# Kernel tuning notes

Hardware: AMD Instinct MI355X
Metric: run time of the kernel (lower is better)

## Reference

```python
import jax, jax.numpy as jnp
import numpy as np

DIM = 1024
N_HEADS = 16
HEAD_DIM = DIM // N_HEADS
MAX_CTX = 2048


def build_rope_cache(seq_len, head_dim, base=10000.0):
    inv_freq = 1.0 / (base ** (jnp.arange(0, head_dim, 2, dtype=jnp.float32) / head_dim))
    t = jnp.arange(seq_len, dtype=jnp.float32)
    freqs = jnp.einsum('i,j->ij', t, inv_freq)  # [T, head_dim//2]
    return jnp.cos(freqs), jnp.sin(freqs)


def apply_rope(x, cos, sin):
    # x: [B, H, T, D]; interleaved even/odd rotation
    x1 = x[..., 0::2]
    x2 = x[..., 1::2]
    c = cos[None, None, :x.shape[-2], :]
    s = sin[None, None, :x.shape[-2], :]
    rx1 = x1 * c - x2 * s
    rx2 = x1 * s + x2 * c
    return jnp.stack([rx1, rx2], axis=-1).reshape(x.shape)


def setup_inputs() -> dict:
    key = jax.random.key(0)
    k1, k2, k3 = jax.random.split(key, 3)
    B, T = 2, 2048
    x = jax.random.normal(k1, (B, T, DIM), dtype=jnp.float32)
    # torch nn.Linear weight shapes: [out_features, in_features]
    qkv_w = jax.random.normal(k2, (3 * DIM, DIM), dtype=jnp.float32) * (1.0 / np.sqrt(DIM))
    out_w = jax.random.normal(k3, (DIM, DIM), dtype=jnp.float32) * (1.0 / np.sqrt(DIM))
    return {"x": x, "qkv_w": qkv_w, "out_w": out_w}


def reference(x, qkv_w, out_w):
    B, T, C = x.shape
    cos, sin = build_rope_cache(MAX_CTX, HEAD_DIM)
    cos = cos.astype(x.dtype)
    sin = sin.astype(x.dtype)

    qkv = jnp.einsum('btc,dc->btd', x, qkv_w)  # [B, T, 3C]
    qkv = qkv.reshape(B, T, 3, N_HEADS, HEAD_DIM).transpose(2, 0, 3, 1, 4)
    q, k, v = qkv[0], qkv[1], qkv[2]  # each [B, H, T, D]

    q = apply_rope(q, cos, sin)
    k = apply_rope(k, cos, sin)

    scale = 1.0 / np.sqrt(HEAD_DIM)
    scores = jnp.einsum('bhqd,bhkd->bhqk', q, k) * scale  # [B, H, T, T]
    causal = jnp.tril(jnp.ones((T, T), dtype=bool))
    scores = jnp.where(causal[None, None], scores, jnp.finfo(scores.dtype).min)
    attn = jax.nn.softmax(scores, axis=-1)
    y = jnp.einsum('bhqk,bhkd->bhqd', attn, v)  # [B, H, T, D]
    y = y.transpose(0, 2, 1, 3).reshape(B, T, C)
    return jnp.einsum('btc,dc->btd', y, out_w)
```

## Files before the change

kernel.cpp:

```cpp
#include <hip/hip_runtime.h>
#include <hip/hip_bf16.h>
#include <cstdint>
#include <cstddef>

#define B_SZ   2
#define T_CTX  2048
#define DIM_C  1024
#define NHEAD  16
#define HD     64
#define NBH    (B_SZ*NHEAD)

typedef __attribute__((ext_vector_type(8))) short short8;
typedef __attribute__((ext_vector_type(4))) float f32x4;
typedef __attribute__((ext_vector_type(16))) float f32x16;

union BV8 { short8 s; __hip_bfloat16 h[8]; unsigned short u[8]; };
union U32x4 { uint32_t u[4]; short8 s8; };

#define GLD16(gp, lp) \
  __builtin_amdgcn_global_load_lds((const __attribute__((address_space(1))) void*)(gp), \
                                   (__attribute__((address_space(3))) void*)(lp), 16, 0, 0)

__device__ inline uint32_t pkbf(float a, float b) {
  union { __hip_bfloat16 h; unsigned short u; } ua, ub;
  ua.h = __float2bfloat16(a);
  ub.h = __float2bfloat16(b);
  return ((uint32_t)ub.u << 16) | (uint32_t)ua.u;
}

__global__ __launch_bounds__(256) void cvt_all(const float* __restrict__ x,
                                               const float* __restrict__ wq,
                                               const float* __restrict__ wo,
                                               __hip_bfloat16* __restrict__ xb,
                                               __hip_bfloat16* __restrict__ wqb,
                                               __hip_bfloat16* __restrict__ wob) {
  int i = blockIdx.x * 256 + threadIdx.x;
  const float* src;
  __hip_bfloat16* dst;
  int off;
  if (i < 1048576) { src = x; dst = xb; off = i; }
  else if (i < 1835008) { src = wq; dst = wqb; off = i - 1048576; }
  else { src = wo; dst = wob; off = i - 1835008; }
  float4 v = reinterpret_cast<const float4*>(src)[off];
  BV8 o;
  o.h[0] = __float2bfloat16(v.x);
  o.h[1] = __float2bfloat16(v.y);
  o.h[2] = __float2bfloat16(v.z);
  o.h[3] = __float2bfloat16(v.w);
  ushort4 st = { o.u[0], o.u[1], o.u[2], o.u[3] };
  reinterpret_cast<ushort4*>(dst)[off] = st;
}

template <typename OutT>
__global__ __launch_bounds__(256) void gemm_bt(const __hip_bfloat16* __restrict__ A,
                                               const __hip_bfloat16* __restrict__ Bt,
                                               OutT* __restrict__ C,
                                               int M, int N, int K) {
  __shared__ __align__(16) char smem[65536];
  const int tid = threadIdx.x;
  const int w = tid >> 6, l = tid & 63;
  const int l15 = l & 15, l4 = l >> 4;
  const int wr = w >> 1, wc = w & 1;
  const int gx = (int)gridDim.x;
  const int nwg = gx * (int)gridDim.y;
  int lin = (int)blockIdx.y * gx + (int)blockIdx.x;
  lin = (lin & 7) * (nwg >> 3) + (lin >> 3);
  const long bm = (long)(lin / gx) * 128;
  const long bn = (long)(lin % gx) * 128;

  f32x4 acc[4][4] = {};

  const int srow = tid >> 3;
  const int scol = (tid & 7) * 16;
  const int ssw  = scol ^ ((srow & 7) << 4);
  const char* Ab  = (const char*)A;
  const char* Btb = (const char*)Bt;

#define GSTAGE(kt_, buf_)                                                   \
  {                                                                         \
    char* base_ = smem + (buf_) * 32768;                                    \
    _Pragma("unroll")                                                       \
    for (int it = 0; it < 4; ++it) {                                        \
      long arow = bm + it * 32 + srow;                                      \
      GLD16(Ab + (arow * K + (kt_)) * 2 + ssw, base_ + it * 4096 + w * 1024);            \
      long brow = bn + it * 32 + srow;                                      \
      GLD16(Btb + (brow * K + (kt_)) * 2 + ssw, base_ + 16384 + it * 4096 + w * 1024);   \
    }                                                                       \
  }

  GSTAGE(0, 0)

  int cur = 0;
  for (int kt = 0; kt < K; kt += 64) {
    __syncthreads();
    if (kt + 64 < K) GSTAGE(kt + 64, cur ^ 1)
    const char* Ac = smem + cur * 32768;
    const char* Bc = Ac + 16384;
#pragma unroll
    for (int ksub = 0; ksub < 2; ++ksub) {
      short8 aF[4], bF[4];
#pragma unroll
      for (int m = 0; m < 4; ++m) {
        int R = wr * 64 + m * 16 + l15;
        aF[m] = *(const short8*)(Ac + R * 128 + ((ksub * 64 + l4 * 16) ^ ((R & 7) << 4)));
      }
#pragma unroll
      for (int n = 0; n < 4; ++n) {
        int R = wc * 64 + n * 16 + l15;
        bF[n] = *(const short8*)(Bc + R * 128 + ((ksub * 64 + l4 * 16) ^ ((R & 7) << 4)));
      }
#pragma unroll
      for (int m = 0; m < 4; ++m)
#pragma unroll
        for (int n = 0; n < 4; ++n)
          acc[m][n] = __builtin_amdgcn_mfma_f32_16x16x32_bf16(aF[m], bF[n], acc[m][n], 0, 0, 0);
    }
    cur ^= 1;
  }
#undef GSTAGE

#pragma unroll
  for (int m = 0; m < 4; ++m)
#pragma unroll
    for (int n = 0; n < 4; ++n)
#pragma unroll
      for (int r = 0; r < 4; ++r) {
        long row = bm + wr * 64 + m * 16 + l4 * 4 + r;
        long col = bn + wc * 64 + n * 16 + l15;
        float v = acc[m][n][r];
        if constexpr (sizeof(OutT) == 2) {
          C[row * N + col] = __float2bfloat16(v);
        } else {
          C[row * N + col] = v;
        }
      }
}

__global__ __launch_bounds__(256) void rope_pack(const __hip_bfloat16* __restrict__ qkv,
                                                 __hip_bfloat16* __restrict__ Qb,
                                                 __hip_bfloat16* __restrict__ Kb,
                                                 __hip_bfloat16* __restrict__ VTb) {
  __shared__ __hip_bfloat16 vt[64][72];
  const int bh = blockIdx.x;
  const int b = bh >> 4, h = bh & 15;
  const int t0 = blockIdx.y * 64;
  const int tid = threadIdx.x;
  const float QSCL = 0.125f * 1.4426950408889634f;

#pragma unroll
  for (int rep = 0; rep < 2; ++rep) {
    int idx = rep * 256 + tid;
    int tt = idx >> 3;
    int d0 = (idx & 7) * 8;
    int t = t0 + tt;
    size_t src = ((size_t)(b * T_CTX + t)) * 3072 + h * 64 + d0;
    BV8 qv, kv, vv, qo, ko;
    qv.s = *(const short8*)(qkv + src);
    kv.s = *(const short8*)(qkv + src + 1024);
    vv.s = *(const short8*)(qkv + src + 2048);
#pragma unroll
    for (int p = 0; p < 4; ++p) {
      int i = (d0 >> 1) + p;
      float inv = exp2f(-13.287712379549449f * ((float)(2 * i) * (1.0f / 64.0f)));
      float ang = (float)t * inv;
      float sn, cn;
      sincosf(ang, &sn, &cn);
      float q1 = __bfloat162float(qv.h[2 * p]);
      float q2 = __bfloat162float(qv.h[2 * p + 1]);
      float k1 = __bfloat162float(kv.h[2 * p]);
      float k2 = __bfloat162float(kv.h[2 * p + 1]);
      qo.h[2 * p]     = __float2bfloat16((q1 * cn - q2 * sn) * QSCL);
      qo.h[2 * p + 1] = __float2bfloat16((q1 * sn + q2 * cn) * QSCL);
      ko.h[2 * p]     = __float2bfloat16(k1 * cn - k2 * sn);
      ko.h[2 * p + 1] = __float2bfloat16(k1 * sn + k2 * cn);
    }
    size_t dst = ((size_t)bh * T_CTX + t) * 64 + d0;
    *(short8*)(Qb + dst) = qo.s;
    *(short8*)(Kb + dst) = ko.s;
#pragma unroll
    for (int j = 0; j < 8; ++j) vt[d0 + j][tt] = vv.h[j];
  }
  __syncthreads();
#pragma unroll
  for (int rep = 0; rep < 2; ++rep) {
    int idx = rep * 256 + tid;
    int d = idx >> 3;
    int toff = (idx & 7) * 8;
    BV8 o;
#pragma unroll
    for (int j = 0; j < 8; ++j) o.h[j] = vt[d][toff + j];
    *(short8*)(VTb + ((size_t)bh * 64 + d) * T_CTX + t0 + toff) = o.s;
  }
}

__global__ __launch_bounds__(256) void flash_attn(const __hip_bfloat16* __restrict__ Qb,
                                                  const __hip_bfloat16* __restrict__ Kb,
                                                  const __hip_bfloat16* __restrict__ VTb,
                                                  __hip_bfloat16* __restrict__ Y) {
  __shared__ __align__(16) char smem[65536];
  const int bh = blockIdx.x;
  const int b = bh >> 4, h = bh & 15;
  const int y = blockIdx.y;
  const int jA = 31 - y;
  const int jB = y;
  const int tid = threadIdx.x;
  const int w = tid >> 6, l = tid & 63;
  const int qsub = w >> 1, kh = w & 1;
  const int l31 = l & 31, hh = l >> 5;
  const int sw7 = (l31 & 7) << 4;
  const int rowb = tid >> 3;
  const int colS = (tid & 7) * 16;

#define STAGE1(gg)                                                                     \
  {                                                                                    \
    const int tt_ = ((gg) <= jA) ? (gg) : (gg) - jA - 1;                               \
    const int kv0_ = tt_ << 6;                                                         \
    char* base_ = smem + (((gg) >> 1) & 1) * 32768 + ((gg) & 1) * 16384;               \
    _Pragma("unroll")                                                                  \
    for (int rnd = 0; rnd < 2; ++rnd) {                                                \
      int row = rnd * 32 + rowb;                                                       \
      int sw = colS ^ ((row & 7) << 4);                                                \
      GLD16((const char*)Kb + (((size_t)bh * T_CTX + kv0_ + row) << 7) + sw,           \
            base_ + rnd * 4096 + w * 1024);                                            \
      GLD16((const char*)VTb + ((((size_t)bh * 64 + row) * T_CTX + kv0_) << 1) + sw,   \
            base_ + 8192 + rnd * 4096 + w * 1024);                                     \
    }                                                                                  \
  }

  f32x16 oA0 = {}, oA1 = {}, oB0 = {}, oB1 = {};
  float lrA = 0.0f, lrB = 0.0f;

  STAGE1(0)
  STAGE1(1)

  int rr = 0;
#pragma unroll
  for (int ph = 0; ph < 2; ++ph) {
    const int j = ph ? jB : jA;
    const int qglob = j * 64 + qsub * 32 + l31;
    f32x16& od0 = ph ? oB0 : oA0;
    f32x16& od1 = ph ? oB1 : oA1;
    float& lrw = ph ? lrB : lrA;

    short8 qB[4];
#pragma unroll
    for (int dblk = 0; dblk < 4; ++dblk)
      qB[dblk] = *(const short8*)(Qb + ((size_t)bh * T_CTX + qglob) * 64 + dblk * 16 + hh * 8);

    for (int t = 0; t <= j; ++t, ++rr) {
      if ((rr & 1) == 0) {
        __syncthreads();
        if (rr + 2 <= 32) STAGE1(rr + 2)
        if (rr + 3 <= 32) STAGE1(rr + 3)
      }
      const char* KsB = smem + ((rr >> 1) & 1) * 32768 + (rr & 1) * 16384;
      const char* VsB = KsB + 8192;
      const int kv0 = t << 6;
      const bool lastT = (t == j);

      if (!(lastT && kh > qsub)) {
        short8 kA[4];
#pragma unroll
        for (int dblk = 0; dblk < 4; ++dblk)
          kA[dblk] = *(const short8*)(KsB + (kh * 32 + l31) * 128 + ((dblk * 32 + hh * 16) ^ sw7));
        short8 vA[2][2];
#pragma unroll
        for (int dt = 0; dt < 2; ++dt)
#pragma unroll
          for (int ks = 0; ks < 2; ++ks)
            vA[dt][ks] = *(const short8*)(VsB + (dt * 32 + l31) * 128 +
                                          ((kh * 64 + ks * 32 + hh * 16) ^ sw7));

        f32x16 sT = {};
#pragma unroll
        for (int dblk = 0; dblk < 4; ++dblk) {
          __builtin_amdgcn_s_setprio(1);
          sT = __builtin_amdgcn_mfma_f32_32x32x16_bf16(kA[dblk], qB[dblk], sT, 0, 0, 0);
          __builtin_amdgcn_s_setprio(0);
        }
        if (lastT && kh == qsub) {
          const int kbase = kv0 + kh * 32 + 4 * hh;
#pragma unroll
          for (int r = 0; r < 16; ++r) {
            int kg = kbase + (r & 3) + 8 * (r >> 2);
            sT[r] = (kg > qglob) ? -1e30f : sT[r];
          }
        }
        float s8[8];
#pragma unroll
        for (int i = 0; i < 8; ++i) {
          sT[i]     = __builtin_amdgcn_exp2f(sT[i]);
          sT[i + 8] = __builtin_amdgcn_exp2f(sT[i + 8]);
          s8[i] = sT[i] + sT[i + 8];
        }
        float ps = ((s8[0] + s8[1]) + (s8[2] + s8[3])) + ((s8[4] + s8[5]) + (s8[6] + s8[7]));
        ps += __shfl_xor(ps, 32);
        lrw += ps;
        uint32_t wk[8];
#pragma unroll
        for (int i = 0; i < 8; ++i) wk[i] = pkbf(sT[2 * i], sT[2 * i + 1]);
#pragma unroll
        for (int ks = 0; ks < 2; ++ks) {
          const int base = ks * 4;
          uint32_t own0 = wk[base + 0], own1 = wk[base + 1];
          uint32_t own2 = wk[base + 2], own3 = wk[base + 3];
          uint32_t e0 = (uint32_t)__shfl_xor((int)(hh ? own0 : own2), 32);
          uint32_t e1 = (uint32_t)__shfl_xor((int)(hh ? own1 : own3), 32);
          U32x4 u;
          u.u[0] = hh ? e0 : own0;
          u.u[1] = hh ? e1 : own1;
          u.u[2] = hh ? own2 : e0;
          u.u[3] = hh ? own3 : e1;
          __builtin_amdgcn_s_setprio(1);
          od0 = __builtin_amdgcn_mfma_f32_32x32x16_bf16(vA[0][ks], u.s8, od0, 0, 0, 0);
          od1 = __builtin_amdgcn_mfma_f32_32x32x16_bf16(vA[1][ks], u.s8, od1, 0, 0, 0);
          __builtin_amdgcn_s_setprio(0);
        }
      }
    }
  }

  __syncthreads();
  {
    float* exch = (float*)smem;
    float* lst = exch + 8192;
    const int slotA = (0 * 2 + qsub) * 2 + kh;
    const int slotB = (1 * 2 + qsub) * 2 + kh;
    const f32x16& nA = kh ? oA0 : oA1;
    const f32x16& nB = kh ? oB0 : oB1;
#pragma unroll
    for (int m = 0; m < 4; ++m) {
      int c = ((2 * m + hh) ^ (l31 & 7)) * 4;
      f32x4 va, vb;
#pragma unroll
      for (int i = 0; i < 4; ++i) { va[i] = nA[m * 4 + i]; vb[i] = nB[m * 4 + i]; }
      *(f32x4*)(exch + slotA * 1024 + l31 * 32 + c) = va;
      *(f32x4*)(exch + slotB * 1024 + l31 * 32 + c) = vb;
    }
    if (hh == 0) {
      lst[slotA * 32 + l31] = lrA;
      lst[slotB * 32 + l31] = lrB;
    }
    __syncthreads();
    const int pA = (0 * 2 + qsub) * 2 + (kh ^ 1);
    const int pB = (1 * 2 + qsub) * 2 + (kh ^ 1);
    float ltA = lrA + lst[pA * 32 + l31];
    float ltB = lrB + lst[pB * 32 + l31];
    f32x16& ownA = kh ? oA1 : oA0;
    f32x16& ownB = kh ? oB1 : oB0;
#pragma unroll
    for (int m = 0; m < 4; ++m) {
      int c = ((2 * m + hh) ^ (l31 & 7)) * 4;
      f32x4 aA = *(const f32x4*)(exch + pA * 1024 + l31 * 32 + c);
      f32x4 aB = *(const f32x4*)(exch + pB * 1024 + l31 * 32 + c);
#pragma unroll
      for (int i = 0; i < 4; ++i) { ownA[m * 4 + i] += aA[i]; ownB[m * 4 + i] += aB[i]; }
    }
#pragma unroll
    for (int sl = 0; sl < 2; ++sl) {
      const f32x16& ov = sl ? ownB : ownA;
      float inv = 1.0f / (sl ? ltB : ltA);
      int q0s = (sl ? jB : jA) * 64 + qsub * 32;
      size_t rowoff = ((size_t)(b * T_CTX + q0s + l31)) * DIM_C + h * 64 + kh * 32;
#pragma unroll
      for (int m = 0; m < 4; ++m) {
        union { ushort4 v; unsigned short us[4]; } st;
#pragma unroll
        for (int i = 0; i < 4; ++i) {
          union { __hip_bfloat16 h2; unsigned short u; } cv;
          cv.h2 = __float2bfloat16(ov[m * 4 + i] * inv);
          st.us[i] = cv.u;
        }
        *(ushort4*)(Y + rowoff + 8 * m + 4 * hh) = st.v;
      }
    }
  }
#undef STAGE1
}

extern "C" void kernel_launch(void* const* d_in, const int* in_sizes, int n_in,
                              void* d_out, int out_size, void* d_ws, size_t ws_size,
                              hipStream_t stream) {
  const float* x     = (const float*)d_in[0];
  const float* qkv_w = (const float*)d_in[1];
  const float* out_w = (const float*)d_in[2];
  float* out = (float*)d_out;

  char* ws = (char*)d_ws;
  const size_t MB = 1024 * 1024;
  __hip_bfloat16* xb    = (__hip_bfloat16*)(ws + 0 * MB);
  __hip_bfloat16* wqkvb = (__hip_bfloat16*)(ws + 8 * MB);
  __hip_bfloat16* woutb = (__hip_bfloat16*)(ws + 14 * MB);
  __hip_bfloat16* qkvb  = (__hip_bfloat16*)(ws + 16 * MB);
  __hip_bfloat16* Qb    = (__hip_bfloat16*)(ws + 40 * MB);
  __hip_bfloat16* Kb    = (__hip_bfloat16*)(ws + 48 * MB);
  __hip_bfloat16* VTb   = (__hip_bfloat16*)(ws + 56 * MB);
  __hip_bfloat16* yb    = (__hip_bfloat16*)(ws + 64 * MB);

  cvt_all<<<8192, 256, 0, stream>>>(x, qkv_w, out_w, xb, wqkvb, woutb);

  gemm_bt<__hip_bfloat16><<<dim3(24, 32), 256, 0, stream>>>(xb, wqkvb, qkvb, 4096, 3072, 1024);

  rope_pack<<<dim3(32, 32), 256, 0, stream>>>(qkvb, Qb, Kb, VTb);

  flash_attn<<<dim3(NBH, 16), 256, 0, stream>>>(Qb, Kb, VTb, yb);

  gemm_bt<float><<<dim3(8, 32), 256, 0, stream>>>(yb, woutb, out, 4096, 1024, 1024);
}
```

Measured before the change: 107.1 us.

## Template GEMM on N-tile width, use BK=32 stages and 128x64 tiles for out-proj

```diff
diff --git a/kernel.cpp b/kernel.cpp
--- a/kernel.cpp
+++ b/kernel.cpp
@@ -51,12 +51,15 @@
   reinterpret_cast<ushort4*>(dst)[off] = st;
 }
 
-template <typename OutT>
+template <typename OutT, int BN>
 __global__ __launch_bounds__(256) void gemm_bt(const __hip_bfloat16* __restrict__ A,
                                                const __hip_bfloat16* __restrict__ Bt,
                                                OutT* __restrict__ C,
                                                int M, int N, int K) {
-  __shared__ __align__(16) char smem[65536];
+  constexpr int NB = BN / 32;
+  constexpr int ABYT = 128 * 64;
+  constexpr int BBYT = BN * 64;
+  __shared__ __align__(16) char smem[2 * (ABYT + BBYT)];
   const int tid = threadIdx.x;
   const int w = tid >> 6, l = tid & 63;
   const int l15 = l & 15, l4 = l >> 4;
@@ -66,55 +69,51 @@
   int lin = (int)blockIdx.y * gx + (int)blockIdx.x;
   lin = (lin & 7) * (nwg >> 3) + (lin >> 3);
   const long bm = (long)(lin / gx) * 128;
-  const long bn = (long)(lin % gx) * 128;
-
-  f32x4 acc[4][4] = {};
-
-  const int srow = tid >> 3;
-  const int scol = (tid & 7) * 16;
-  const int ssw  = scol ^ ((srow & 7) << 4);
+  const long bn = (long)(lin % gx) * BN;
+
+  f32x4 acc[4][NB] = {};
+
+  const int srow = tid >> 2;
+  const int scol = (tid & 3) * 16;
   const char* Ab  = (const char*)A;
   const char* Btb = (const char*)Bt;
 
-#define GSTAGE(kt_, buf_)                                                   \
-  {                                                                         \
-    char* base_ = smem + (buf_) * 32768;                                    \
-    _Pragma("unroll")                                                       \
-    for (int it = 0; it < 4; ++it) {                                        \
-      long arow = bm + it * 32 + srow;                                      \
-      GLD16(Ab + (arow * K + (kt_)) * 2 + ssw, base_ + it * 4096 + w * 1024);            \
-      long brow = bn + it * 32 + srow;                                      \
-      GLD16(Btb + (brow * K + (kt_)) * 2 + ssw, base_ + 16384 + it * 4096 + w * 1024);   \
-    }                                                                       \
+#define GSTAGE(kt_, buf_)                                                        \
+  {                                                                              \
+    char* base_ = smem + (buf_) * (ABYT + BBYT);                                 \
+    _Pragma("unroll")                                                            \
+    for (int it = 0; it < 2; ++it) {                                             \
+      long arow = bm + it * 64 + srow;                                           \
+      GLD16(Ab + (arow * K + (kt_)) * 2 + scol, base_ + it * 4096 + w * 1024);   \
+    }                                                                            \
+    _Pragma("unroll")                                                            \
+    for (int it = 0; it < BN / 64; ++it) {                                       \
+      long brow = bn + it * 64 + srow;                                           \
+      GLD16(Btb + (brow * K + (kt_)) * 2 + scol,                                 \
+            base_ + ABYT + it * 4096 + w * 1024);                                \
+    }                                                                            \
   }
 
   GSTAGE(0, 0)
 
   int cur = 0;
-  for (int kt = 0; kt < K; kt += 64) {
+  for (int kt = 0; kt < K; kt += 32) {
     __syncthreads();
-    if (kt + 64 < K) GSTAGE(kt + 64, cur ^ 1)
-    const char* Ac = smem + cur * 32768;
-    const char* Bc = Ac + 16384;
-#pragma unroll
-    for (int ksub = 0; ksub < 2; ++ksub) {
-      short8 aF[4], bF[4];
-#pragma unroll
-      for (int m = 0; m < 4; ++m) {
-        int R = wr * 64 + m * 16 + l15;
-        aF[m] = *(const short8*)(Ac + R * 128 + ((ksub * 64 + l4 * 16) ^ ((R & 7) << 4)));
-      }
-#pragma unroll
-      for (int n = 0; n < 4; ++n) {
-        int R = wc * 64 + n * 16 + l15;
-        bF[n] = *(const short8*)(Bc + R * 128 + ((ksub * 64 + l4 * 16) ^ ((R & 7) << 4)));
-      }
-#pragma unroll
-      for (int m = 0; m < 4; ++m)
-#pragma unroll
-        for (int n = 0; n < 4; ++n)
-          acc[m][n] = __builtin_amdgcn_mfma_f32_16x16x32_bf16(aF[m], bF[n], acc[m][n], 0, 0, 0);
-    }
+    if (kt + 32 < K) GSTAGE(kt + 32, cur ^ 1)
+    const char* Ac = smem + cur * (ABYT + BBYT);
+    const char* Bc = Ac + ABYT;
+    short8 aF[4], bF[NB];
+#pragma unroll
+    for (int m = 0; m < 4; ++m)
+      aF[m] = *(const short8*)(Ac + (wr * 64 + m * 16 + l15) * 64 + l4 * 16);
+#pragma unroll
+    for (int n = 0; n < NB; ++n)
+      bF[n] = *(const short8*)(Bc + (wc * (BN / 2) + n * 16 + l15) * 64 + l4 * 16);
+#pragma unroll
+    for (int m = 0; m < 4; ++m)
+#pragma unroll
+      for (int n = 0; n < NB; ++n)
+        acc[m][n] = __builtin_amdgcn_mfma_f32_16x16x32_bf16(aF[m], bF[n], acc[m][n], 0, 0, 0);
     cur ^= 1;
   }
 #undef GSTAGE
@@ -122,11 +121,11 @@
 #pragma unroll
   for (int m = 0; m < 4; ++m)
 #pragma unroll
-    for (int n = 0; n < 4; ++n)
+    for (int n = 0; n < NB; ++n)
 #pragma unroll
       for (int r = 0; r < 4; ++r) {
         long row = bm + wr * 64 + m * 16 + l4 * 4 + r;
-        long col = bn + wc * 64 + n * 16 + l15;
+        long col = bn + wc * (BN / 2) + n * 16 + l15;
         float v = acc[m][n][r];
         if constexpr (sizeof(OutT) == 2) {
           C[row * N + col] = __float2bfloat16(v);
@@ -399,11 +398,11 @@
 
   cvt_all<<<8192, 256, 0, stream>>>(x, qkv_w, out_w, xb, wqkvb, woutb);
 
-  gemm_bt<__hip_bfloat16><<<dim3(24, 32), 256, 0, stream>>>(xb, wqkvb, qkvb, 4096, 3072, 1024);
+  gemm_bt<__hip_bfloat16, 128><<<dim3(24, 32), 256, 0, stream>>>(xb, wqkvb, qkvb, 4096, 3072, 1024);
 
   rope_pack<<<dim3(32, 32), 256, 0, stream>>>(qkvb, Qb, Kb, VTb);
 
   flash_attn<<<dim3(NBH, 16), 256, 0, stream>>>(Qb, Kb, VTb, yb);
 
-  gemm_bt<float><<<dim3(8, 32), 256, 0, stream>>>(yb, woutb, out, 4096, 1024, 1024);
-}
+  gemm_bt<float, 64><<<dim3(16, 32), 256, 0, stream>>>(yb, woutb, out, 4096, 1024, 1024);
+}
```

Result: slower. 110.7 us (+3.4%).
